# Optimization experiments

Hardware: AMD Instinct MI355X
Metric: run time of the kernel (lower is better)

Reference implementation:

```python
import jax, jax.numpy as jnp
import numpy as np

N = 8192
E = 262144
D_IN = 128
D_OUT = 128


def setup_inputs() -> dict:
    key = jax.random.key(0)
    k1, k2, k3, k4 = jax.random.split(key, 4)
    x = jax.random.normal(k1, (N, D_IN), dtype=jnp.float32)
    edge_index = jax.random.randint(k2, (2, E), 0, N, dtype=jnp.int64)
    # Linear(in_channels, out_channels) params (Kaiming-uniform-ish init scale)
    bound = 1.0 / np.sqrt(D_IN)
    W = jax.random.uniform(k3, (D_OUT, D_IN), minval=-bound, maxval=bound, dtype=jnp.float32)
    b = jax.random.uniform(k4, (D_OUT,), minval=-bound, maxval=bound, dtype=jnp.float32)
    return {"x": x, "edge_index": edge_index, "W": W, "b": b}


def reference(x, edge_index, W, b):
    num_nodes = x.shape[0]
    # Dense adjacency via scatter-set (duplicates collapse to 1, like torch assignment)
    adjacency = jnp.zeros((num_nodes, num_nodes), dtype=x.dtype)
    adjacency = adjacency.at[edge_index[0], edge_index[1]].set(1.0)
    adjacency = adjacency + jnp.eye(num_nodes, dtype=x.dtype)
    degree = adjacency.sum(axis=1, keepdims=True)  # [N,1]
    norm = jnp.where(degree > 0, degree ** -0.5, jnp.zeros_like(degree))
    norm = norm * norm.T  # [N,N] symmetric normalization
    norm = norm * adjacency
    h = x @ W.T + b  # [N, D_OUT]
    out = norm @ h
    return out
```

## Files before the change

kernel.cpp:

```cpp
#include <hip/hip_runtime.h>
#include <hip/hip_fp16.h>
#include <cstdint>
#include <cstddef>

#define NN 8192
#define DD 128
#define RCAP 96

__global__ __launch_bounds__(256) void scatter_kernel(const int* __restrict__ ei, int E,
                                                      int* __restrict__ cnt,
                                                      int* __restrict__ adj) {
    int e = blockIdx.x * blockDim.x + threadIdx.x;
    if (e >= E) return;
    int src = ei[e];
    int dst = ei[E + e];
    if ((unsigned)src < (unsigned)NN && (unsigned)dst < (unsigned)NN) {
        int pos = atomicAdd(&cnt[src], 1);
        if (pos < RCAP) adj[(size_t)src * RCAP + pos] = dst;
    }
}

__global__ __launch_bounds__(256) void dedup_kernel(const int* __restrict__ cnt,
                                                    const int* __restrict__ adj,
                                                    int* __restrict__ uadj,
                                                    int* __restrict__ ucnt,
                                                    float* __restrict__ dinv) {
    __shared__ unsigned bm[4][256];
    const int tid = threadIdx.x;
    const int lane = tid & 63;
    const int wave = tid >> 6;
    const int row = blockIdx.x * 4 + wave;

    bm[wave][lane]       = 0u;
    bm[wave][lane + 64]  = 0u;
    bm[wave][lane + 128] = 0u;
    bm[wave][lane + 192] = 0u;
    __syncthreads();

    int rc = cnt[row]; if (rc > RCAP) rc = RCAP;
    for (int k = lane; k < rc; k += 64) {
        int dst = adj[(size_t)row * RCAP + k];
        atomicOr(&bm[wave][dst >> 5], 1u << (dst & 31));
    }
    __syncthreads();

    unsigned w0 = bm[wave][lane * 4 + 0];
    unsigned w1 = bm[wave][lane * 4 + 1];
    unsigned w2 = bm[wave][lane * 4 + 2];
    unsigned w3 = bm[wave][lane * 4 + 3];
    int c = __popc(w0) + __popc(w1) + __popc(w2) + __popc(w3);
    int scan = c;
    #pragma unroll
    for (int off = 1; off < 64; off <<= 1) {
        int o = __shfl_up(scan, off);
        if (lane >= off) scan += o;
    }
    int pos = row * RCAP + (scan - c);
    const int b0 = lane * 128;
    unsigned ws[4] = {w0, w1, w2, w3};
    #pragma unroll
    for (int q = 0; q < 4; ++q) {
        unsigned w = ws[q];
        while (w) {
            int bb = __ffs(w) - 1;
            w &= w - 1;
            uadj[pos++] = b0 + q * 32 + bb;
        }
    }
    if (lane == 63) {
        ucnt[row] = scan;
        dinv[row] = rsqrtf((float)(scan + 1));
    }
}

__global__ __launch_bounds__(64) void linear_kernel(const float* __restrict__ x,
                                                    const float* __restrict__ Wm,
                                                    const float* __restrict__ bias,
                                                    int* __restrict__ cnt,
                                                    __half* __restrict__ h) {
    if (blockIdx.x < 128) cnt[blockIdx.x * 64 + threadIdx.x] = 0;

    __shared__ float Wl[32][36];
    __shared__ float xl[32][36];
    const int tid = threadIdx.x;
    const int row0 = (blockIdx.x >> 2) * 32;
    const int c0   = (blockIdx.x & 3) * 32;
    const int d4 = tid & 7;
    const int rg = tid >> 3;

    float acc[4][4];
    #pragma unroll
    for (int r = 0; r < 4; ++r)
        #pragma unroll
        for (int c = 0; c < 4; ++c) acc[r][c] = 0.0f;

    for (int kt = 0; kt < 4; ++kt) {
        #pragma unroll
        for (int i = tid; i < 1024; i += 64) {
            int o = i >> 5, kk = i & 31;
            Wl[kk][o] = Wm[(size_t)(c0 + o) * DD + kt * 32 + kk];
        }
        #pragma unroll
        for (int i = tid; i < 1024; i += 64) {
            int r = i >> 5, kk = i & 31;
            xl[kk][r] = x[(size_t)(row0 + r) * DD + kt * 32 + kk];
        }
        __syncthreads();
        #pragma unroll 8
        for (int kk = 0; kk < 32; ++kk) {
            const float4 w4 = *(const float4*)&Wl[kk][d4 * 4];
            const float4 x4 = *(const float4*)&xl[kk][rg * 4];
            acc[0][0] += x4.x * w4.x; acc[0][1] += x4.x * w4.y; acc[0][2] += x4.x * w4.z; acc[0][3] += x4.x * w4.w;
            acc[1][0] += x4.y * w4.x; acc[1][1] += x4.y * w4.y; acc[1][2] += x4.y * w4.z; acc[1][3] += x4.y * w4.w;
            acc[2][0] += x4.z * w4.x; acc[2][1] += x4.z * w4.y; acc[2][2] += x4.z * w4.z; acc[2][3] += x4.z * w4.w;
            acc[3][0] += x4.w * w4.x; acc[3][1] += x4.w * w4.y; acc[3][2] += x4.w * w4.z; acc[3][3] += x4.w * w4.w;
        }
        __syncthreads();
    }

    const float4 b4 = *(const float4*)&bias[c0 + d4 * 4];
    #pragma unroll
    for (int r = 0; r < 4; ++r) {
        const int row = row0 + rg * 4 + r;
        float4 o;
        o.x = acc[r][0] + b4.x;
        o.y = acc[r][1] + b4.y;
        o.z = acc[r][2] + b4.z;
        o.w = acc[r][3] + b4.w;
        union { uint2 u; __half2 hh[2]; } pk;
        pk.hh[0] = __floats2half2_rn(o.x, o.y);
        pk.hh[1] = __floats2half2_rn(o.z, o.w);
        *(uint2*)&h[(size_t)row * DD + c0 + d4 * 4] = pk.u;
    }
}

__global__ __launch_bounds__(256) void agg_kernel(const int* __restrict__ ucnt,
                                                  const int* __restrict__ uadj,
                                                  const float* __restrict__ dinv,
                                                  const __half* __restrict__ h,
                                                  float* __restrict__ out) {
    __shared__ int nl[RCAP];
    __shared__ float nd[RCAP];
    __shared__ float4 red[8][32];
    const int i = blockIdx.x;
    const int tid = threadIdx.x;
    const int u = ucnt[i];
    if (tid < u) {
        int j = uadj[(size_t)i * RCAP + tid];
        nl[tid] = j;
        nd[tid] = dinv[j];
    }
    __syncthreads();

    const int sub = tid >> 5;
    const int d4 = tid & 31;
    const uint2* hp = (const uint2*)h;
    float4 a0 = make_float4(0.f, 0.f, 0.f, 0.f);
    float4 a1 = make_float4(0.f, 0.f, 0.f, 0.f);
    float4 a2 = make_float4(0.f, 0.f, 0.f, 0.f);
    float4 a3 = make_float4(0.f, 0.f, 0.f, 0.f);
    int k = sub;
    for (; k + 24 < u; k += 32) {
        int j0 = nl[k], j1 = nl[k + 8], j2 = nl[k + 16], j3 = nl[k + 24];
        float s0 = nd[k], s1 = nd[k + 8], s2 = nd[k + 16], s3 = nd[k + 24];
        union { uint2 uu; __half2 hh[2]; } c0_, c1_, c2_, c3_;
        c0_.uu = hp[(size_t)j0 * 32 + d4];
        c1_.uu = hp[(size_t)j1 * 32 + d4];
        c2_.uu = hp[(size_t)j2 * 32 + d4];
        c3_.uu = hp[(size_t)j3 * 32 + d4];
        float2 f0a = __half22float2(c0_.hh[0]), f0b = __half22float2(c0_.hh[1]);
        float2 f1a = __half22float2(c1_.hh[0]), f1b = __half22float2(c1_.hh[1]);
        float2 f2a = __half22float2(c2_.hh[0]), f2b = __half22float2(c2_.hh[1]);
        float2 f3a = __half22float2(c3_.hh[0]), f3b = __half22float2(c3_.hh[1]);
        a0.x += s0 * f0a.x; a0.y += s0 * f0a.y; a0.z += s0 * f0b.x; a0.w += s0 * f0b.y;
        a1.x += s1 * f1a.x; a1.y += s1 * f1a.y; a1.z += s1 * f1b.x; a1.w += s1 * f1b.y;
        a2.x += s2 * f2a.x; a2.y += s2 * f2a.y; a2.z += s2 * f2b.x; a2.w += s2 * f2b.y;
        a3.x += s3 * f3a.x; a3.y += s3 * f3a.y; a3.z += s3 * f3b.x; a3.w += s3 * f3b.y;
    }
    for (; k < u; k += 8) {
        float s0 = nd[k];
        union { uint2 uu; __half2 hh[2]; } c0_;
        c0_.uu = hp[(size_t)nl[k] * 32 + d4];
        float2 f0a = __half22float2(c0_.hh[0]), f0b = __half22float2(c0_.hh[1]);
        a0.x += s0 * f0a.x; a0.y += s0 * f0a.y; a0.z += s0 * f0b.x; a0.w += s0 * f0b.y;
    }
    a0.x += a1.x + a2.x + a3.x;
    a0.y += a1.y + a2.y + a3.y;
    a0.z += a1.z + a2.z + a3.z;
    a0.w += a1.w + a2.w + a3.w;
    red[sub][d4] = a0;
    __syncthreads();

    if (tid < 128) {
        const float* redf = (const float*)red;
        float s = 0.f;
        #pragma unroll
        for (int q = 0; q < 8; ++q) s += redf[q * 128 + tid];
        const float di = dinv[i];
        const float hv = __half2float(h[(size_t)i * DD + tid]);
        out[(size_t)i * DD + tid] = di * (s + di * hv);
    }
}

extern "C" void kernel_launch(void* const* d_in, const int* in_sizes, int n_in,
                              void* d_out, int out_size, void* d_ws, size_t ws_size,
                              hipStream_t stream) {
    const float* x  = (const float*)d_in[0];
    const int*   ei = (const int*)d_in[1];
    const float* Wm = (const float*)d_in[2];
    const float* bs = (const float*)d_in[3];
    float* out = (float*)d_out;
    const int E = in_sizes[1] / 2;

    char* p = (char*)d_ws;
    int* cnt    = (int*)p;   p += (size_t)NN * sizeof(int);
    int* ucnt   = (int*)p;   p += (size_t)NN * sizeof(int);
    float* dinv = (float*)p; p += (size_t)NN * sizeof(float);
    int* adj    = (int*)p;   p += (size_t)NN * RCAP * sizeof(int);
    int* uadj   = (int*)p;   p += (size_t)NN * RCAP * sizeof(int);
    __half* h   = (__half*)p;

    linear_kernel<<<1024, 64, 0, stream>>>(x, Wm, bs, cnt, h);
    scatter_kernel<<<(E + 255) / 256, 256, 0, stream>>>(ei, E, cnt, adj);
    dedup_kernel<<<NN / 4, 256, 0, stream>>>(cnt, adj, uadj, ucnt, dinv);
    agg_kernel<<<NN, 256, 0, stream>>>(ucnt, uadj, dinv, h, out);
}
```

Measured before the change: 52.81 us.

## Aggregate one row per wavefront with shuffle-broadcast neighbor lists

The aggregation kernel now assigns one node row to each 64-lane wavefront (4 rows per block) instead of one row per 256-thread block. Neighbor indices and degree scales are held in registers and broadcast with __shfl, which removes the shared-memory staging, both __syncthreads and the cross-wave reduction. Each lane gathers a half2 per neighbor, so there are fewer lanes in flight per row but each wave walks the whole neighbor list serially.

```diff
diff --git a/kernel.cpp b/kernel.cpp
--- a/kernel.cpp
+++ b/kernel.cpp
@@ -139,67 +139,61 @@
                                                   const float* __restrict__ dinv,
                                                   const __half* __restrict__ h,
                                                   float* __restrict__ out) {
-    __shared__ int nl[RCAP];
-    __shared__ float nd[RCAP];
-    __shared__ float4 red[8][32];
-    const int i = blockIdx.x;
-    const int tid = threadIdx.x;
-    const int u = ucnt[i];
-    if (tid < u) {
-        int j = uadj[(size_t)i * RCAP + tid];
-        nl[tid] = j;
-        nd[tid] = dinv[j];
-    }
-    __syncthreads();
-
-    const int sub = tid >> 5;
-    const int d4 = tid & 31;
-    const uint2* hp = (const uint2*)h;
-    float4 a0 = make_float4(0.f, 0.f, 0.f, 0.f);
-    float4 a1 = make_float4(0.f, 0.f, 0.f, 0.f);
-    float4 a2 = make_float4(0.f, 0.f, 0.f, 0.f);
-    float4 a3 = make_float4(0.f, 0.f, 0.f, 0.f);
-    int k = sub;
-    for (; k + 24 < u; k += 32) {
-        int j0 = nl[k], j1 = nl[k + 8], j2 = nl[k + 16], j3 = nl[k + 24];
-        float s0 = nd[k], s1 = nd[k + 8], s2 = nd[k + 16], s3 = nd[k + 24];
-        union { uint2 uu; __half2 hh[2]; } c0_, c1_, c2_, c3_;
-        c0_.uu = hp[(size_t)j0 * 32 + d4];
-        c1_.uu = hp[(size_t)j1 * 32 + d4];
-        c2_.uu = hp[(size_t)j2 * 32 + d4];
-        c3_.uu = hp[(size_t)j3 * 32 + d4];
-        float2 f0a = __half22float2(c0_.hh[0]), f0b = __half22float2(c0_.hh[1]);
-        float2 f1a = __half22float2(c1_.hh[0]), f1b = __half22float2(c1_.hh[1]);
-        float2 f2a = __half22float2(c2_.hh[0]), f2b = __half22float2(c2_.hh[1]);
-        float2 f3a = __half22float2(c3_.hh[0]), f3b = __half22float2(c3_.hh[1]);
-        a0.x += s0 * f0a.x; a0.y += s0 * f0a.y; a0.z += s0 * f0b.x; a0.w += s0 * f0b.y;
-        a1.x += s1 * f1a.x; a1.y += s1 * f1a.y; a1.z += s1 * f1b.x; a1.w += s1 * f1b.y;
-        a2.x += s2 * f2a.x; a2.y += s2 * f2a.y; a2.z += s2 * f2b.x; a2.w += s2 * f2b.y;
-        a3.x += s3 * f3a.x; a3.y += s3 * f3a.y; a3.z += s3 * f3b.x; a3.w += s3 * f3b.y;
-    }
-    for (; k < u; k += 8) {
-        float s0 = nd[k];
-        union { uint2 uu; __half2 hh[2]; } c0_;
-        c0_.uu = hp[(size_t)nl[k] * 32 + d4];
-        float2 f0a = __half22float2(c0_.hh[0]), f0b = __half22float2(c0_.hh[1]);
-        a0.x += s0 * f0a.x; a0.y += s0 * f0a.y; a0.z += s0 * f0b.x; a0.w += s0 * f0b.y;
-    }
-    a0.x += a1.x + a2.x + a3.x;
-    a0.y += a1.y + a2.y + a3.y;
-    a0.z += a1.z + a2.z + a3.z;
-    a0.w += a1.w + a2.w + a3.w;
-    red[sub][d4] = a0;
-    __syncthreads();
-
-    if (tid < 128) {
-        const float* redf = (const float*)red;
-        float s = 0.f;
-        #pragma unroll
-        for (int q = 0; q < 8; ++q) s += redf[q * 128 + tid];
-        const float di = dinv[i];
-        const float hv = __half2float(h[(size_t)i * DD + tid]);
-        out[(size_t)i * DD + tid] = di * (s + di * hv);
-    }
+    const int lane = threadIdx.x & 63;
+    const int wave = threadIdx.x >> 6;
+    const int row = blockIdx.x * 4 + wave;
+    const int u = ucnt[row];
+
+    int nl0 = 0, nl1 = 0;
+    float nd0 = 0.f, nd1 = 0.f;
+    if (lane < u) { nl0 = uadj[(size_t)row * RCAP + lane]; nd0 = dinv[nl0]; }
+    const int u1 = u - 64;
+    if (lane < u1) { nl1 = uadj[(size_t)row * RCAP + 64 + lane]; nd1 = dinv[nl1]; }
+
+    const __half2* h2 = (const __half2*)h;
+    float2 a0 = make_float2(0.f, 0.f);
+    float2 a1 = make_float2(0.f, 0.f);
+    float2 a2 = make_float2(0.f, 0.f);
+    float2 a3 = make_float2(0.f, 0.f);
+
+    const int kmax = (u < 64) ? u : 64;
+    int k = 0;
+    for (; k + 3 < kmax; k += 4) {
+        int j0 = __shfl(nl0, k),     j1 = __shfl(nl0, k + 1);
+        int j2 = __shfl(nl0, k + 2), j3 = __shfl(nl0, k + 3);
+        float s0 = __shfl(nd0, k),     s1 = __shfl(nd0, k + 1);
+        float s2 = __shfl(nd0, k + 2), s3 = __shfl(nd0, k + 3);
+        float2 v0 = __half22float2(h2[(size_t)j0 * 64 + lane]);
+        float2 v1 = __half22float2(h2[(size_t)j1 * 64 + lane]);
+        float2 v2 = __half22float2(h2[(size_t)j2 * 64 + lane]);
+        float2 v3 = __half22float2(h2[(size_t)j3 * 64 + lane]);
+        a0.x += s0 * v0.x; a0.y += s0 * v0.y;
+        a1.x += s1 * v1.x; a1.y += s1 * v1.y;
+        a2.x += s2 * v2.x; a2.y += s2 * v2.y;
+        a3.x += s3 * v3.x; a3.y += s3 * v3.y;
+    }
+    for (; k < kmax; ++k) {
+        int j0 = __shfl(nl0, k);
+        float s0 = __shfl(nd0, k);
+        float2 v0 = __half22float2(h2[(size_t)j0 * 64 + lane]);
+        a0.x += s0 * v0.x; a0.y += s0 * v0.y;
+    }
+    for (k = 64; k < u; ++k) {
+        int j0 = __shfl(nl1, k - 64);
+        float s0 = __shfl(nd1, k - 64);
+        float2 v0 = __half22float2(h2[(size_t)j0 * 64 + lane]);
+        a0.x += s0 * v0.x; a0.y += s0 * v0.y;
+    }
+
+    float2 acc;
+    acc.x = (a0.x + a1.x) + (a2.x + a3.x);
+    acc.y = (a0.y + a1.y) + (a2.y + a3.y);
+    const float di = dinv[row];
+    float2 hv = __half22float2(h2[(size_t)row * 64 + lane]);
+    float2 o;
+    o.x = di * (acc.x + di * hv.x);
+    o.y = di * (acc.y + di * hv.y);
+    *(float2*)&out[(size_t)row * DD + lane * 2] = o;
 }
 
 extern "C" void kernel_launch(void* const* d_in, const int* in_sizes, int n_in,
@@ -223,5 +217,5 @@
     linear_kernel<<<1024, 64, 0, stream>>>(x, Wm, bs, cnt, h);
     scatter_kernel<<<(E + 255) / 256, 256, 0, stream>>>(ei, E, cnt, adj);
     dedup_kernel<<<NN / 4, 256, 0, stream>>>(cnt, adj, uadj, ucnt, dinv);
-    agg_kernel<<<NN, 256, 0, stream>>>(ucnt, uadj, dinv, h, out);
-}
+    agg_kernel<<<NN / 4, 256, 0, stream>>>(ucnt, uadj, dinv, h, out);
+}
```

Result: faster. 48.78 us (-7.6%).
